# Performance work log

Hardware: AMD Instinct MI355X
Metric: run time of the kernel (lower is better)

## Reference

```python
import jax, jax.numpy as jnp
import numpy as np

B, L, C, H, FF = 2, 2048, 1024, 16, 4096
HD = C // H
SCALE = HD ** -0.5
EPS = 1e-5


def _ln(x, g, b):
    m = jnp.mean(x, axis=-1, keepdims=True)
    v = jnp.mean((x - m) ** 2, axis=-1, keepdims=True)
    return (x - m) * jax.lax.rsqrt(v + EPS) * g + b


def setup_inputs() -> dict:
    key = jax.random.key(0)
    ks = jax.random.split(key, 12)
    s = lambda fan_in: 1.0 / np.sqrt(fan_in)
    return {
        "x": jax.random.normal(ks[0], (B, L, C), jnp.float32),
        "freq_diff": jax.random.normal(ks[1], (B, L), jnp.float32),
        "qkv_w": jax.random.normal(ks[2], (C, 3 * C), jnp.float32) * s(C),
        "qkv_b": jnp.zeros((3 * C,), jnp.float32),
        "fp_w1": jax.random.normal(ks[3], (1, C), jnp.float32),
        "fp_b1": jnp.zeros((C,), jnp.float32),
        "fp_ln_g": jnp.ones((C,), jnp.float32),
        "fp_ln_b": jnp.zeros((C,), jnp.float32),
        "fp_w2": jax.random.normal(ks[4], (C, C), jnp.float32) * s(C),
        "fp_b2": jnp.zeros((C,), jnp.float32),
        "wq_w": jax.random.normal(ks[5], (HD, HD), jnp.float32) * s(HD),
        "wq_b": jnp.zeros((HD,), jnp.float32),
        "wk_w": jax.random.normal(ks[6], (HD, HD), jnp.float32) * s(HD),
        "wk_b": jnp.zeros((HD,), jnp.float32),
        "out_w": jax.random.normal(ks[7], (C, C), jnp.float32) * s(C),
        "out_b": jnp.zeros((C,), jnp.float32),
        "n1_g": jnp.ones((C,), jnp.float32),
        "n1_b": jnp.zeros((C,), jnp.float32),
        "n2_g": jnp.ones((C,), jnp.float32),
        "n2_b": jnp.zeros((C,), jnp.float32),
        "mlp_w1": jax.random.normal(ks[8], (C, FF), jnp.float32) * s(C),
        "mlp_b1": jnp.zeros((FF,), jnp.float32),
        "mlp_w2": jax.random.normal(ks[9], (FF, C), jnp.float32) * s(FF),
        "mlp_b2": jnp.zeros((C,), jnp.float32),
        "freq_scale": jnp.ones((1,), jnp.float32),
    }


def reference(x, freq_diff, qkv_w, qkv_b, fp_w1, fp_b1, fp_ln_g, fp_ln_b,
              fp_w2, fp_b2, wq_w, wq_b, wk_w, wk_b, out_w, out_b,
              n1_g, n1_b, n2_g, n2_b, mlp_w1, mlp_b1, mlp_w2, mlp_b2,
              freq_scale):
    shortcut = x
    xn = _ln(x, n1_g, n1_b)
    qkv = (xn @ qkv_w + qkv_b).reshape(B, L, 3, H, HD)
    qkv = jnp.transpose(qkv, (2, 0, 3, 1, 4))  # [3,B,H,L,HD]
    q, k, v = qkv[0], qkv[1], qkv[2]

    # frequency bias: MLP on scalar freq_diff -> per-head bias vectors
    fb = freq_diff[..., None] @ fp_w1 + fp_b1          # [B,L,C]
    fb = jax.nn.gelu(_ln(fb, fp_ln_g, fp_ln_b), approximate=False)
    fb = fb @ fp_w2 + fp_b2                            # [B,L,C]
    fb = jnp.transpose(fb.reshape(B, L, H, HD), (0, 2, 1, 3))  # [B,H,L,HD]
    qb = fb @ wq_w + wq_b
    kb = fb @ wk_w + wk_b
    freq_attn_bias = jnp.einsum('bhqd,bhkd->bhqk', qb, kb)

    attn = jnp.einsum('bhqd,bhkd->bhqk', q, k) * SCALE
    attn = attn + freq_scale[0] * freq_attn_bias
    attn = jax.nn.softmax(attn, axis=-1)
    o = jnp.einsum('bhqk,bhkd->bhqd', attn, v)
    o = jnp.transpose(o, (0, 2, 1, 3)).reshape(B, L, C)
    x = shortcut + (o @ out_w + out_b)

    xn2 = _ln(x, n2_g, n2_b)
    h = jax.nn.gelu(xn2 @ mlp_w1 + mlp_b1, approximate=False)
    x = x + (h @ mlp_w2 + mlp_b2)
    return x
```

## Files before the change

kernel.cpp:

```cpp
#include <hip/hip_runtime.h>
#include <math.h>


typedef __bf16 bf16;
typedef float f32x4 __attribute__((ext_vector_type(4)));
typedef bf16 bf16x8 __attribute__((ext_vector_type(8)));
typedef bf16 bf16x4 __attribute__((ext_vector_type(4)));

#define DEVINL __device__ __forceinline__

#define LOG2E 1.4426950408889634f

DEVINL float fast_exp2(float x) { return __builtin_amdgcn_exp2f(x); }

DEVINL void async_load16(const void* g, void* l) {
  __builtin_amdgcn_global_load_lds(
      (const __attribute__((address_space(1))) unsigned int*)g,
      (__attribute__((address_space(3))) unsigned int*)l, 16, 0, 0);
}

DEVINL f32x4 mfma16(bf16x8 a, bf16x8 b, f32x4 c) {
  return __builtin_amdgcn_mfma_f32_16x16x32_bf16(a, b, c, 0, 0, 0);
}

DEVINL float gelu_exact(float v) {
  return 0.5f * v * (1.0f + erff(v * 0.70710678118654752f));
}

DEVINL void block_reduce2(float& a, float& b, float* red, int tid) {
#pragma unroll
  for (int off = 32; off >= 1; off >>= 1) {
    a += __shfl_xor(a, off);
    b += __shfl_xor(b, off);
  }
  int w = tid >> 6;
  if ((tid & 63) == 0) { red[2 * w] = a; red[2 * w + 1] = b; }
  __syncthreads();
  a = red[0] + red[2] + red[4] + red[6];
  b = red[1] + red[3] + red[5] + red[7];
  __syncthreads();
}

__global__ __launch_bounds__(256) void transpose_cast(
    const float* __restrict__ W, bf16* __restrict__ Wt, int K, int N) {
  __shared__ float tile[32][33];
  int n0 = blockIdx.x * 32, k0 = blockIdx.y * 32;
  int tx = threadIdx.x & 31, ty = threadIdx.x >> 5;
#pragma unroll
  for (int r = 0; r < 4; ++r)
    tile[ty + r * 8][tx] = W[(size_t)(k0 + ty + r * 8) * N + n0 + tx];
  __syncthreads();
#pragma unroll
  for (int r = 0; r < 4; ++r)
    Wt[(size_t)(n0 + ty + r * 8) * K + k0 + tx] = (bf16)tile[tx][ty + r * 8];
}

__global__ __launch_bounds__(256) void prec_qk(
    const float* __restrict__ fp_w2, const float* __restrict__ fp_b2,
    const float* __restrict__ wq_w, const float* __restrict__ wq_b,
    const float* __restrict__ wk_w, const float* __restrict__ wk_b,
    bf16* __restrict__ wqk2t, float* __restrict__ bqk) {
  __shared__ float Wl[64 * 64];
  __shared__ float Al[64 * 128];
  const int id = blockIdx.x;
  const int sel = id >> 7, h = (id >> 3) & 15, ck = id & 7;
  const int t = threadIdx.x;
  const float* wsel = sel ? wk_w : wq_w;
#pragma unroll
  for (int i = 0; i < 4; ++i)
    ((float4*)Wl)[i * 256 + t] = ((const float4*)wsel)[i * 256 + t];
  const int c0 = ck * 128, off = h * 64;
#pragma unroll
  for (int it = 0; it < 8; ++it) {
    int idx = it * 256 + t;
    int rr = idx >> 4, c4 = idx & 15;
    float4 v = *(const float4*)(fp_w2 + (size_t)(c0 + rr) * 1024 + off + c4 * 4);
    float vv[4] = {v.x, v.y, v.z, v.w};
#pragma unroll
    for (int k = 0; k < 4; ++k) {
      int i2 = c4 * 4 + k;
      Al[i2 * 128 + (rr ^ (i2 & 31))] = vv[k];
    }
  }
  __syncthreads();
  const int cr = t & 127, jh = (t >> 7) * 32;
  float acc[32];
#pragma unroll
  for (int j = 0; j < 32; ++j) acc[j] = 0.f;
  for (int i = 0; i < 64; ++i) {
    float a = Al[i * 128 + (cr ^ (i & 31))];
    const float4* wrow = (const float4*)(Wl + i * 64 + jh);
#pragma unroll
    for (int j4 = 0; j4 < 8; ++j4) {
      float4 wv = wrow[j4];
      acc[j4 * 4 + 0] += a * wv.x;
      acc[j4 * 4 + 1] += a * wv.y;
      acc[j4 * 4 + 2] += a * wv.z;
      acc[j4 * 4 + 3] += a * wv.w;
    }
  }
  const int nbase = sel * 1024 + off + jh;
#pragma unroll
  for (int j = 0; j < 32; ++j)
    wqk2t[(size_t)(nbase + j) * 1024 + c0 + cr] = (bf16)acc[j];
  if (ck == 0 && t < 64) {
    float s = 0.f;
    for (int i = 0; i < 64; ++i) s += fp_b2[off + i] * Wl[i * 64 + t];
    bqk[sel * 1024 + off + t] = s + (sel ? wk_b[t] : wq_b[t]);
  }
}

__global__ __launch_bounds__(256) void ln1_kernel(
    const float* __restrict__ x, const float* __restrict__ fd,
    const float* __restrict__ g1, const float* __restrict__ b1,
    const float* __restrict__ fw1, const float* __restrict__ fb1,
    const float* __restrict__ flg, const float* __restrict__ flb,
    bf16* __restrict__ xn, bf16* __restrict__ gout) {
  __shared__ float red[8];
  int tok = blockIdx.x, t = threadIdx.x;
  float4 xv = ((const float4*)(x + (size_t)tok * 1024))[t];
  float s = xv.x + xv.y + xv.z + xv.w;
  float ss = xv.x * xv.x + xv.y * xv.y + xv.z * xv.z + xv.w * xv.w;
  block_reduce2(s, ss, red, t);
  float mean = s * (1.0f / 1024.0f);
  float rsig = rsqrtf(ss * (1.0f / 1024.0f) - mean * mean + 1e-5f);
  float4 g4 = ((const float4*)g1)[t], b4 = ((const float4*)b1)[t];
  bf16x4 o;
  o[0] = (bf16)((xv.x - mean) * rsig * g4.x + b4.x);
  o[1] = (bf16)((xv.y - mean) * rsig * g4.y + b4.y);
  o[2] = (bf16)((xv.z - mean) * rsig * g4.z + b4.z);
  o[3] = (bf16)((xv.w - mean) * rsig * g4.w + b4.w);
  ((bf16x4*)xn)[(size_t)tok * 256 + t] = o;

  float dv = fd[tok];
  float4 w4 = ((const float4*)fw1)[t], c4 = ((const float4*)fb1)[t];
  float f0 = dv * w4.x + c4.x, f1 = dv * w4.y + c4.y;
  float f2 = dv * w4.z + c4.z, f3 = dv * w4.w + c4.w;
  s = f0 + f1 + f2 + f3;
  ss = f0 * f0 + f1 * f1 + f2 * f2 + f3 * f3;
  block_reduce2(s, ss, red, t);
  mean = s * (1.0f / 1024.0f);
  rsig = rsqrtf(ss * (1.0f / 1024.0f) - mean * mean + 1e-5f);
  float4 lg = ((const float4*)flg)[t], lb = ((const float4*)flb)[t];
  bf16x4 q;
  q[0] = (bf16)gelu_exact((f0 - mean) * rsig * lg.x + lb.x);
  q[1] = (bf16)gelu_exact((f1 - mean) * rsig * lg.y + lb.y);
  q[2] = (bf16)gelu_exact((f2 - mean) * rsig * lg.z + lb.z);
  q[3] = (bf16)gelu_exact((f3 - mean) * rsig * lg.w + lb.w);
  ((bf16x4*)gout)[(size_t)tok * 256 + t] = q;
}

__global__ __launch_bounds__(256) void ln_kernel(
    const float* __restrict__ xin, const float* __restrict__ g,
    const float* __restrict__ b, bf16* __restrict__ xout) {
  __shared__ float red[8];
  int tok = blockIdx.x, t = threadIdx.x;
  float4 xv = ((const float4*)(xin + (size_t)tok * 1024))[t];
  float s = xv.x + xv.y + xv.z + xv.w;
  float ss = xv.x * xv.x + xv.y * xv.y + xv.z * xv.z + xv.w * xv.w;
  block_reduce2(s, ss, red, t);
  float mean = s * (1.0f / 1024.0f);
  float rsig = rsqrtf(ss * (1.0f / 1024.0f) - mean * mean + 1e-5f);
  float4 g4 = ((const float4*)g)[t], b4 = ((const float4*)b)[t];
  bf16x4 o;
  o[0] = (bf16)((xv.x - mean) * rsig * g4.x + b4.x);
  o[1] = (bf16)((xv.y - mean) * rsig * g4.y + b4.y);
  o[2] = (bf16)((xv.z - mean) * rsig * g4.z + b4.z);
  o[3] = (bf16)((xv.w - mean) * rsig * g4.w + b4.w);
  ((bf16x4*)xout)[(size_t)tok * 256 + t] = o;
}

template <class Epi>
__global__ __launch_bounds__(256) void gemm_bf16_k(
    const bf16* __restrict__ A, const bf16* __restrict__ Bt,
    int M, int N, int K, Epi epi) {
  __shared__ bf16 As[2][128 * 32];
  __shared__ bf16 Bs[2][128 * 32];
  const int tid = threadIdx.x;
  const int lane = tid & 63, w = tid >> 6;
  const int quad = lane >> 4, lm = lane & 15;
  const int wm = w >> 1, wn = w & 1;
  const int m0 = blockIdx.y * 128, n0 = blockIdx.x * 128;

  f32x4 acc[4][4];
#pragma unroll
  for (int i = 0; i < 4; ++i)
#pragma unroll
    for (int j = 0; j < 4; ++j) {
      acc[i][j][0] = 0.f; acc[i][j][1] = 0.f; acc[i][j][2] = 0.f; acc[i][j][3] = 0.f;
    }

  const bf16* Ag = A + (size_t)m0 * K;
  const bf16* Bg = Bt + (size_t)n0 * K;

  auto stage = [&](int k0, int buf) {
#pragma unroll
    for (int i = 0; i < 2; ++i) {
      int ch = i * 256 + tid, r = ch >> 2, c = ch & 3;
      async_load16(Ag + (size_t)r * K + k0 + c * 8,
                   (char*)As[buf] + (i * 256 + w * 64) * 16);
      async_load16(Bg + (size_t)r * K + k0 + c * 8,
                   (char*)Bs[buf] + (i * 256 + w * 64) * 16);
    }
  };

  stage(0, 0);
  const int nk = K >> 5;
  for (int ki = 0; ki < nk; ++ki) {
    __syncthreads();
    if (ki + 1 < nk) stage((ki + 1) << 5, (ki + 1) & 1);
    const bf16* Ac = As[ki & 1];
    const bf16* Bc = Bs[ki & 1];
    bf16x8 af[4], bfv[4];
#pragma unroll
    for (int mi = 0; mi < 4; ++mi)
      af[mi] = *(const bf16x8*)(Ac + (wm * 64 + mi * 16 + lm) * 32 + quad * 8);
#pragma unroll
    for (int ni = 0; ni < 4; ++ni)
      bfv[ni] = *(const bf16x8*)(Bc + (wn * 64 + ni * 16 + lm) * 32 + quad * 8);
#pragma unroll
    for (int mi = 0; mi < 4; ++mi)
#pragma unroll
      for (int ni = 0; ni < 4; ++ni)
        acc[mi][ni] = mfma16(af[mi], bfv[ni], acc[mi][ni]);
  }

#pragma unroll
  for (int mi = 0; mi < 4; ++mi)
#pragma unroll
    for (int ni = 0; ni < 4; ++ni)
      epi(m0 + wm * 64 + mi * 16 + quad * 4, n0 + wn * 64 + ni * 16 + lm, acc[mi][ni]);
}

__global__ __launch_bounds__(256) void gemm_mlp2_part(
    const bf16* __restrict__ A, const bf16* __restrict__ Bt,
    float* __restrict__ part) {
  __shared__ bf16 As[2][128 * 32];
  __shared__ bf16 Bs[2][128 * 32];
  const int tid = threadIdx.x;
  const int lane = tid & 63, w = tid >> 6;
  const int quad = lane >> 4, lm = lane & 15;
  const int wm = w >> 1, wn = w & 1;
  const int id = blockIdx.x;
  const int kz = id & 3;
  const int n0 = ((id >> 2) & 7) * 128;
  const int m0 = (id >> 5) * 128;

  f32x4 acc[4][4];
#pragma unroll
  for (int i = 0; i < 4; ++i)
#pragma unroll
    for (int j = 0; j < 4; ++j) {
      acc[i][j][0] = 0.f; acc[i][j][1] = 0.f; acc[i][j][2] = 0.f; acc[i][j][3] = 0.f;
    }

  const bf16* Ag = A + (size_t)m0 * 4096 + kz * 1024;
  const bf16* Bg = Bt + (size_t)n0 * 4096 + kz * 1024;

  auto stage = [&](int k0, int buf) {
#pragma unroll
    for (int i = 0; i < 2; ++i) {
      int ch = i * 256 + tid, r = ch >> 2, c = ch & 3;
      async_load16(Ag + (size_t)r * 4096 + k0 + c * 8,
                   (char*)As[buf] + (i * 256 + w * 64) * 16);
      async_load16(Bg + (size_t)r * 4096 + k0 + c * 8,
                   (char*)Bs[buf] + (i * 256 + w * 64) * 16);
    }
  };

  stage(0, 0);
  for (int ki = 0; ki < 32; ++ki) {
    __syncthreads();
    if (ki + 1 < 32) stage((ki + 1) << 5, (ki + 1) & 1);
    const bf16* Ac = As[ki & 1];
    const bf16* Bc = Bs[ki & 1];
    bf16x8 af[4], bfv[4];
#pragma unroll
    for (int mi = 0; mi < 4; ++mi)
      af[mi] = *(const bf16x8*)(Ac + (wm * 64 + mi * 16 + lm) * 32 + quad * 8);
#pragma unroll
    for (int ni = 0; ni < 4; ++ni)
      bfv[ni] = *(const bf16x8*)(Bc + (wn * 64 + ni * 16 + lm) * 32 + quad * 8);
#pragma unroll
    for (int mi = 0; mi < 4; ++mi)
#pragma unroll
      for (int ni = 0; ni < 4; ++ni)
        acc[mi][ni] = mfma16(af[mi], bfv[ni], acc[mi][ni]);
  }

  float* dst = part + (size_t)kz * 4096 * 1024;
#pragma unroll
  for (int mi = 0; mi < 4; ++mi)
#pragma unroll
    for (int ni = 0; ni < 4; ++ni) {
      int row = m0 + wm * 64 + mi * 16 + quad * 4;
      int col = n0 + wn * 64 + ni * 16 + lm;
#pragma unroll
      for (int r = 0; r < 4; ++r)
        dst[(size_t)(row + r) * 1024 + col] = acc[mi][ni][r];
    }
}

__global__ __launch_bounds__(256) void reduce_mlp2(
    const float* __restrict__ part, float* __restrict__ out) {
  size_t i = (size_t)blockIdx.x * 256 + threadIdx.x;
  const float4* p = (const float4*)part;
  float4 o = ((const float4*)out)[i];
  const size_t S = (size_t)4096 * 256;
  float4 a = p[i], b = p[i + S], c = p[i + 2 * S], d = p[i + 3 * S];
  o.x += a.x + b.x + c.x + d.x;
  o.y += a.y + b.y + c.y + d.y;
  o.z += a.z + b.z + c.z + d.z;
  o.w += a.w + b.w + c.w + d.w;
  ((float4*)out)[i] = o;
}

struct EpiQKV {
  const float* __restrict__ bias;
  bf16 *Qc, *Kc, *Vt;
  DEVINL void operator()(int row, int col, f32x4 v) const {
    int b = row >> 11, l = row & 2047;
    float bia = bias[col];
    if (col < 1024) {
      int h = col >> 6, d = col & 63;
      bf16* p = Qc + (size_t)(((b << 4) + h) * 2048 + l) * 128 + d;
#pragma unroll
      for (int r = 0; r < 4; ++r) p[r * 128] = (bf16)((v[r] + bia) * (0.125f * LOG2E));
    } else if (col < 2048) {
      int c2 = col - 1024, h = c2 >> 6, d = c2 & 63;
      bf16* p = Kc + (size_t)(((b << 4) + h) * 2048 + l) * 128 + d;
#pragma unroll
      for (int r = 0; r < 4; ++r) p[r * 128] = (bf16)(v[r] + bia);
    } else {
      int c2 = col - 2048, h = c2 >> 6, d = c2 & 63;
      bf16x4 pk;
#pragma unroll
      for (int r = 0; r < 4; ++r) pk[r] = (bf16)(v[r] + bia);
      *(bf16x4*)(Vt + (size_t)(((b << 4) + h) * 64 + d) * 2048 + l) = pk;
    }
  }
};

struct EpiQBKB {
  const float* __restrict__ bias;
  const float* __restrict__ fs;
  bf16 *Qc, *Kc;
  DEVINL void operator()(int row, int col, f32x4 v) const {
    int b = row >> 11, l = row & 2047;
    float bia = bias[col];
    if (col < 1024) {
      int h = col >> 6, d = col & 63;
      float sc = fs[0] * LOG2E;
      bf16* p = Qc + (size_t)(((b << 4) + h) * 2048 + l) * 128 + 64 + d;
#pragma unroll
      for (int r = 0; r < 4; ++r) p[r * 128] = (bf16)((v[r] + bia) * sc);
    } else {
      int c2 = col - 1024, h = c2 >> 6, d = c2 & 63;
      bf16* p = Kc + (size_t)(((b << 4) + h) * 2048 + l) * 128 + 64 + d;
#pragma unroll
      for (int r = 0; r < 4; ++r) p[r * 128] = (bf16)(v[r] + bia);
    }
  }
};

struct EpiOut {
  const float* __restrict__ bias;
  const float* __restrict__ x;
  const float* __restrict__ b2;
  float* x1;
  float* out0;
  DEVINL void operator()(int row, int col, f32x4 v) const {
    float bia = bias[col];
    float b2v = b2[col];
#pragma unroll
    for (int r = 0; r < 4; ++r) {
      size_t idx = (size_t)(row + r) * 1024 + col;
      float xv = x[idx] + v[r] + bia;
      x1[idx] = xv;
      out0[idx] = xv + b2v;
    }
  }
};

struct EpiMLP1 {
  const float* __restrict__ bias;
  bf16* hbf;
  DEVINL void operator()(int row, int col, f32x4 v) const {
    float bia = bias[col];
#pragma unroll
    for (int r = 0; r < 4; ++r)
      hbf[(size_t)(row + r) * 4096 + col] = (bf16)gelu_exact(v[r] + bia);
  }
};

__global__ __launch_bounds__(512, 4) void flash_kernel(
    const bf16* __restrict__ Qc, const bf16* __restrict__ Kcp,
    const bf16* __restrict__ Vt, bf16* __restrict__ Obf) {
  __shared__ bf16 KsA[64 * 128];
  __shared__ bf16 KsB[64 * 128];
  __shared__ bf16 VsA[64 * 64];
  __shared__ bf16 VsB[64 * 64];
  __shared__ bf16 Ps[128 * 64];

  const int tid = threadIdx.x, lane = tid & 63, w = tid >> 6;
  const int quad = lane >> 4, lm = lane & 15;
  const int id = blockIdx.x;
  const int bh = id & 31, qt = id >> 5;
  const int b = bh >> 4, h = bh & 15;

  const bf16* Qg = Qc + ((size_t)bh * 2048 + qt * 128) * 128;
#pragma unroll
  for (int i = 0; i < 4; ++i) {
    int ch = i * 512 + tid, r = ch >> 4, cs = ch & 15, c = cs ^ (r & 7);
    char* dst = (i < 2) ? (char*)KsA + (i * 512 + w * 64) * 16
                        : (char*)KsB + ((i - 2) * 512 + w * 64) * 16;
    async_load16(Qg + (size_t)r * 128 + c * 8, dst);
  }
  __syncthreads();
  const int qr = w * 16 + lm;
  bf16x8 qf[4];
  {
    const bf16* base = (w < 4) ? KsA : KsB;
    int rr = qr & 63;
#pragma unroll
    for (int ks = 0; ks < 4; ++ks) {
      int pos = (ks * 4 + quad) ^ (lm & 7);
      qf[ks] = *(const bf16x8*)(base + rr * 128 + pos * 8);
    }
  }
  __syncthreads();

  float m_run = -3.0e38f, l_run = 0.f;
  f32x4 o_acc[4];
#pragma unroll
  for (int nf = 0; nf < 4; ++nf) {
    o_acc[nf][0] = 0.f; o_acc[nf][1] = 0.f; o_acc[nf][2] = 0.f; o_acc[nf][3] = 0.f;
  }

  const bf16* Kg0 = Kcp + (size_t)bh * 2048 * 128;
  const bf16* Vg0 = Vt + (size_t)bh * 64 * 2048;

  auto stage = [&](int kv, bf16* Kdst, bf16* Vdst) {
    const bf16* Kg = Kg0 + (size_t)kv * 64 * 128;
#pragma unroll
    for (int i = 0; i < 2; ++i) {
      int ch = i * 512 + tid, key = ch >> 4, c = (ch & 15) ^ (key & 7);
      async_load16(Kg + (size_t)key * 128 + c * 8,
                   (char*)Kdst + (i * 512 + w * 64) * 16);
    }
    {
      int d = tid >> 3, c = (tid & 7) ^ (d & 7);
      async_load16(Vg0 + (size_t)d * 2048 + kv * 64 + c * 8,
                   (char*)Vdst + (w * 64) * 16);
    }
  };

  stage(0, KsA, VsA);

  for (int kv = 0; kv < 32; ++kv) {
    const bf16* Kcur = (kv & 1) ? KsB : KsA;
    const bf16* Vcur = (kv & 1) ? VsB : VsA;
    __syncthreads();
    if (kv + 1 < 32)
      stage(kv + 1, (kv & 1) ? KsA : KsB, (kv & 1) ? VsA : VsB);

    f32x4 sa[4];
#pragma unroll
    for (int nk = 0; nk < 4; ++nk) {
      sa[nk][0] = 0.f; sa[nk][1] = 0.f; sa[nk][2] = 0.f; sa[nk][3] = 0.f;
    }
#pragma unroll
    for (int ks = 0; ks < 4; ++ks) {
      bf16x8 ak[4];
#pragma unroll
      for (int nk = 0; nk < 4; ++nk) {
        int key = nk * 16 + lm;
        int pos = (ks * 4 + quad) ^ (key & 7);
        ak[nk] = *(const bf16x8*)(Kcur + key * 128 + pos * 8);
      }
#pragma unroll
      for (int nk = 0; nk < 4; ++nk)
        sa[nk] = mfma16(ak[nk], qf[ks], sa[nk]);
    }

    float mx = sa[0][0];
#pragma unroll
    for (int nk = 0; nk < 4; ++nk)
#pragma unroll
      for (int rg = 0; rg < 4; ++rg) mx = fmaxf(mx, sa[nk][rg]);
    mx = fmaxf(mx, __shfl_xor(mx, 16));
    mx = fmaxf(mx, __shfl_xor(mx, 32));
    float mnew = fmaxf(m_run, mx);
    float alpha = fast_exp2(m_run - mnew);
    m_run = mnew;
    float rs = 0.f;
#pragma unroll
    for (int nk = 0; nk < 4; ++nk)
#pragma unroll
      for (int rg = 0; rg < 4; ++rg) {
        float pv = fast_exp2(sa[nk][rg] - mnew);
        sa[nk][rg] = pv;
        rs += pv;
      }
    rs += __shfl_xor(rs, 16);
    rs += __shfl_xor(rs, 32);
    l_run = l_run * alpha + rs;
#pragma unroll
    for (int nf = 0; nf < 4; ++nf) {
      o_acc[nf][0] *= alpha; o_acc[nf][1] *= alpha;
      o_acc[nf][2] *= alpha; o_acc[nf][3] *= alpha;
    }

#pragma unroll
    for (int nk = 0; nk < 4; ++nk) {
      int c16 = 2 * nk + (quad >> 1);
      int cs = c16 ^ (lm & 7);
      bf16x4 pk;
      pk[0] = (bf16)sa[nk][0]; pk[1] = (bf16)sa[nk][1];
      pk[2] = (bf16)sa[nk][2]; pk[3] = (bf16)sa[nk][3];
      *(bf16x4*)(Ps + qr * 64 + cs * 8 + (quad & 1) * 4) = pk;
    }

#pragma unroll
    for (int ks = 0; ks < 2; ++ks) {
      bf16x8 pa, vb[4];
      {
        int cs = (ks * 4 + quad) ^ (lm & 7);
        pa = *(const bf16x8*)(Ps + qr * 64 + cs * 8);
      }
#pragma unroll
      for (int nf = 0; nf < 4; ++nf) {
        int d = nf * 16 + lm;
        int cs = (ks * 4 + quad) ^ (d & 7);
        vb[nf] = *(const bf16x8*)(Vcur + d * 64 + cs * 8);
      }
#pragma unroll
      for (int nf = 0; nf < 4; ++nf)
        o_acc[nf] = mfma16(vb[nf], pa, o_acc[nf]);
    }
  }

  float inv = 1.0f / l_run;
  int l = qt * 128 + qr;
#pragma unroll
  for (int nf = 0; nf < 4; ++nf) {
    bf16x4 ov;
#pragma unroll
    for (int rg = 0; rg < 4; ++rg) ov[rg] = (bf16)(o_acc[nf][rg] * inv);
    int d = h * 64 + nf * 16 + quad * 4;
    *(bf16x4*)(Obf + ((size_t)b * 2048 + l) * 1024 + d) = ov;
  }
}

extern "C" void kernel_launch(void* const* d_in, const int* in_sizes, int n_in,
                              void* d_out, int out_size, void* d_ws, size_t ws_size,
                              hipStream_t stream) {
  (void)in_sizes; (void)n_in; (void)out_size; (void)ws_size;
  const float* x      = (const float*)d_in[0];
  const float* fd     = (const float*)d_in[1];
  const float* qkv_w  = (const float*)d_in[2];
  const float* qkv_b  = (const float*)d_in[3];
  const float* fp_w1  = (const float*)d_in[4];
  const float* fp_b1  = (const float*)d_in[5];
  const float* fp_ln_g= (const float*)d_in[6];
  const float* fp_ln_b= (const float*)d_in[7];
  const float* fp_w2  = (const float*)d_in[8];
  const float* fp_b2  = (const float*)d_in[9];
  const float* wq_w   = (const float*)d_in[10];
  const float* wq_b   = (const float*)d_in[11];
  const float* wk_w   = (const float*)d_in[12];
  const float* wk_b   = (const float*)d_in[13];
  const float* out_w  = (const float*)d_in[14];
  const float* out_b  = (const float*)d_in[15];
  const float* n1_g   = (const float*)d_in[16];
  const float* n1_b   = (const float*)d_in[17];
  const float* n2_g   = (const float*)d_in[18];
  const float* n2_b   = (const float*)d_in[19];
  const float* mlp_w1 = (const float*)d_in[20];
  const float* mlp_b1 = (const float*)d_in[21];
  const float* mlp_w2 = (const float*)d_in[22];
  const float* mlp_b2 = (const float*)d_in[23];
  const float* fscale = (const float*)d_in[24];
  float* out = (float*)d_out;

  char* p = (char*)d_ws;
  auto take = [&](size_t n) { char* r = p; p += (n + 255) & ~(size_t)255; return r; };
  bf16* xn_bf  = (bf16*)take((size_t)4096 * 1024 * 2);
  bf16* g_bf   = (bf16*)take((size_t)4096 * 1024 * 2);
  bf16* Qc     = (bf16*)take((size_t)32 * 2048 * 128 * 2);
  bf16* Kc     = (bf16*)take((size_t)32 * 2048 * 128 * 2);
  bf16* Vt     = (bf16*)take((size_t)32 * 64 * 2048 * 2);
  bf16* o_bf   = (bf16*)take((size_t)4096 * 1024 * 2);
  float* x1    = (float*)take((size_t)4096 * 1024 * 4);
  bf16* ln2_bf = (bf16*)take((size_t)4096 * 1024 * 2);
  bf16* h_bf   = (bf16*)take((size_t)4096 * 4096 * 2);
  bf16* qkv_wt = (bf16*)take((size_t)3072 * 1024 * 2);
  bf16* out_wt = (bf16*)take((size_t)1024 * 1024 * 2);
  bf16* w1t    = (bf16*)take((size_t)4096 * 1024 * 2);
  bf16* w2t    = (bf16*)take((size_t)1024 * 4096 * 2);
  bf16* wqk2t  = (bf16*)take((size_t)2048 * 1024 * 2);
  float* bqk   = (float*)take((size_t)2048 * 4);

  float* part = (float*)xn_bf;

  dim3 b256(256);

  transpose_cast<<<dim3(3072 / 32, 1024 / 32), b256, 0, stream>>>(qkv_w, qkv_wt, 1024, 3072);
  transpose_cast<<<dim3(1024 / 32, 1024 / 32), b256, 0, stream>>>(out_w, out_wt, 1024, 1024);
  transpose_cast<<<dim3(4096 / 32, 1024 / 32), b256, 0, stream>>>(mlp_w1, w1t, 1024, 4096);
  transpose_cast<<<dim3(1024 / 32, 4096 / 32), b256, 0, stream>>>(mlp_w2, w2t, 4096, 1024);
  prec_qk<<<dim3(256), b256, 0, stream>>>(fp_w2, fp_b2, wq_w, wq_b, wk_w, wk_b, wqk2t, bqk);

  ln1_kernel<<<dim3(4096), b256, 0, stream>>>(x, fd, n1_g, n1_b, fp_w1, fp_b1,
                                              fp_ln_g, fp_ln_b, xn_bf, g_bf);

  gemm_bf16_k<<<dim3(24, 32), b256, 0, stream>>>(xn_bf, qkv_wt, 4096, 3072, 1024,
                                                 EpiQKV{qkv_b, Qc, Kc, Vt});
  gemm_bf16_k<<<dim3(16, 32), b256, 0, stream>>>(g_bf, wqk2t, 4096, 2048, 1024,
                                                 EpiQBKB{bqk, fscale, Qc, Kc});
  flash_kernel<<<dim3(512), dim3(512), 0, stream>>>(Qc, Kc, Vt, o_bf);

  gemm_bf16_k<<<dim3(8, 32), b256, 0, stream>>>(o_bf, out_wt, 4096, 1024, 1024,
                                                EpiOut{out_b, x, mlp_b2, x1, out});
  ln_kernel<<<dim3(4096), b256, 0, stream>>>(x1, n2_g, n2_b, ln2_bf);
  gemm_bf16_k<<<dim3(32, 32), b256, 0, stream>>>(ln2_bf, w1t, 4096, 4096, 1024,
                                                 EpiMLP1{mlp_b1, h_bf});
  gemm_mlp2_part<<<dim3(1024), b256, 0, stream>>>(h_bf, w2t, part);
  reduce_mlp2<<<dim3(4096), b256, 0, stream>>>(part, out);
}
```

Measured before the change: 513.9 us.

## Add 256x256 ping-pong GEMM with swizzled LDS and use for QKV/MLP GEMMs

Introduces a 512-thread 256x256-tile bf16 GEMM kernel with XOR-swizzled LDS layout, four-phase interleaved async staging, raw barriers with MFMA priority bumps and explicit vmcnt waits, plus block-index swizzling for L2 locality. It replaces the 128x128 GEMMs for QKV, freq-bias QK, MLP1 and split-K MLP2. The goal is higher data reuse per tile, fewer LDS bank conflicts and better overlap of loads with MFMA. In exchange, small grids (128-256 blocks) may underfill the GPU's compute units, and the hand-placed waitcnt sequencing is fragile.

```diff
diff --git a/kernel.cpp b/kernel.cpp
--- a/kernel.cpp
+++ b/kernel.cpp
@@ -25,6 +25,12 @@
 
 DEVINL float gelu_exact(float v) {
   return 0.5f * v * (1.0f + erff(v * 0.70710678118654752f));
+}
+
+DEVINL void hard_barrier() {
+  asm volatile("" ::: "memory");
+  __builtin_amdgcn_s_barrier();
+  asm volatile("" ::: "memory");
 }
 
 DEVINL void block_reduce2(float& a, float& b, float* red, int tid) {
@@ -170,6 +176,131 @@
   ((bf16x4*)xout)[(size_t)tok * 256 + t] = o;
 }
 
+#define PHASE(MH, NH, LA, LB, STAGE_STMT, WAIT_STMT)                          \
+  do {                                                                        \
+    if (LA) {                                                                 \
+      _Pragma("unroll") for (int ml = 0; ml < 4; ++ml) {                      \
+        _Pragma("unroll") for (int ks = 0; ks < 2; ++ks) {                    \
+          const int rr = ml * 16 + lm;                                        \
+          const int cc = (((ks * 4 + quad) ^ (lm & 7)) << 3);                 \
+          af[ml][ks] = *(const bf16x8*)&As[bsel][MH][wm][rr][cc];             \
+        }                                                                     \
+      }                                                                       \
+    }                                                                         \
+    if (LB) {                                                                 \
+      _Pragma("unroll") for (int nl = 0; nl < 2; ++nl) {                      \
+        _Pragma("unroll") for (int ks = 0; ks < 2; ++ks) {                    \
+          const int rr = nl * 16 + lm;                                        \
+          const int cc = (((ks * 4 + quad) ^ (lm & 7)) << 3);                 \
+          bfr[nl][ks] = *(const bf16x8*)&Bs[bsel][NH][wn][rr][cc];            \
+        }                                                                     \
+      }                                                                       \
+    }                                                                         \
+    STAGE_STMT;                                                               \
+    hard_barrier();                                                           \
+    __builtin_amdgcn_s_setprio(1);                                            \
+    _Pragma("unroll") for (int ks = 0; ks < 2; ++ks) {                        \
+      _Pragma("unroll") for (int ml = 0; ml < 4; ++ml) {                      \
+        _Pragma("unroll") for (int nl = 0; nl < 2; ++nl) {                    \
+          acc[(MH)*4 + ml][(NH)*2 + nl] = mfma16(                             \
+              af[ml][ks], bfr[nl][ks], acc[(MH)*4 + ml][(NH)*2 + nl]);        \
+        }                                                                     \
+      }                                                                       \
+    }                                                                         \
+    __builtin_amdgcn_s_setprio(0);                                            \
+    WAIT_STMT;                                                                \
+    hard_barrier();                                                           \
+  } while (0)
+
+template <class Epi>
+__global__ __launch_bounds__(512, 2) void gemm256(
+    const bf16* __restrict__ A, const bf16* __restrict__ Bt,
+    int lda, int ldb, int K, int kstride, int nbx, int nblk, int rowoffz,
+    Epi epi) {
+  __shared__ __align__(16) bf16 As[2][2][2][64][64];
+  __shared__ __align__(16) bf16 Bs[2][2][4][32][64];
+
+  const int tid = threadIdx.x;
+  const int lane = tid & 63, w = tid >> 6;
+  const int quad = lane >> 4, lm = lane & 15;
+  const int wm = w >> 2, wn = w & 3;
+
+  const int kz = blockIdx.x / nblk;
+  const int bid = blockIdx.x - kz * nblk;
+  const int swz = (nblk & 7) ? bid : ((bid & 7) * (nblk >> 3) + (bid >> 3));
+  const int tm = swz / nbx, tn = swz - tm * nbx;
+  const int m0 = tm << 8, n0 = tn << 8;
+  const int rowoff = kz * rowoffz;
+  A += (size_t)kz * kstride;
+  Bt += (size_t)kz * kstride;
+
+  const bf16* Abase = A + (size_t)m0 * lda;
+  const bf16* Bbase = Bt + (size_t)n0 * ldb;
+
+  auto stageA = [&](int b, int mh, int kt) {
+#pragma unroll
+    for (int j = 0; j < 2; ++j) {
+      const int q = (w * 2 + j) * 64 + lane;
+      const int wm2 = q >> 9, rr = (q >> 3) & 63, c = q & 7;
+      async_load16(Abase + (size_t)(wm2 * 128 + mh * 64 + rr) * lda +
+                       (size_t)kt * 64 + ((c ^ (rr & 7)) << 3),
+                   (char*)&As[b][mh][0][0][0] + (w * 2 + j) * 1024);
+    }
+  };
+  auto stageB = [&](int b, int nh, int kt) {
+#pragma unroll
+    for (int j = 0; j < 2; ++j) {
+      const int q = (w * 2 + j) * 64 + lane;
+      const int wn4 = q >> 8, rr = (q >> 3) & 31, c = q & 7;
+      async_load16(Bbase + (size_t)(wn4 * 64 + nh * 32 + rr) * ldb +
+                       (size_t)kt * 64 + ((c ^ (rr & 7)) << 3),
+                   (char*)&Bs[b][nh][0][0][0] + (w * 2 + j) * 1024);
+    }
+  };
+
+  f32x4 acc[8][4];
+#pragma unroll
+  for (int i = 0; i < 8; ++i)
+#pragma unroll
+    for (int j = 0; j < 4; ++j) {
+      acc[i][j][0] = 0.f; acc[i][j][1] = 0.f;
+      acc[i][j][2] = 0.f; acc[i][j][3] = 0.f;
+    }
+  bf16x8 af[4][2], bfr[2][2];
+
+  stageA(0, 0, 0);
+  stageB(0, 1, 0);
+  stageA(0, 1, 0);
+  stageB(0, 0, 0);
+  stageA(1, 0, 1);
+  stageB(1, 1, 1);
+  asm volatile("s_waitcnt vmcnt(4)" ::: "memory");
+  hard_barrier();
+
+  const int nt = K >> 6;
+  int bsel = 0;
+  for (int t = 0; t < nt; ++t, bsel ^= 1) {
+    PHASE(0, 0, 1, 1, { if (t + 1 < nt) stageA(bsel ^ 1, 1, t + 1); }, {});
+    PHASE(0, 1, 0, 1, { if (t + 1 < nt) stageB(bsel ^ 1, 0, t + 1); }, {});
+    PHASE(1, 1, 1, 0, { if (t + 2 < nt) stageA(bsel, 0, t + 2); }, {});
+    PHASE(1, 0, 0, 1, { if (t + 2 < nt) stageB(bsel, 1, t + 2); },
+          {
+            if (t + 2 < nt) {
+              asm volatile("s_waitcnt vmcnt(4)" ::: "memory");
+            } else if (t + 1 < nt) {
+              asm volatile("s_waitcnt vmcnt(0)" ::: "memory");
+            }
+          });
+  }
+
+#pragma unroll
+  for (int mi = 0; mi < 8; ++mi)
+#pragma unroll
+    for (int ni = 0; ni < 4; ++ni)
+      epi(rowoff + m0 + wm * 128 + mi * 16 + quad * 4,
+          n0 + wn * 64 + ni * 16 + lm, acc[mi][ni]);
+}
+
 template <class Epi>
 __global__ __launch_bounds__(256) void gemm_bf16_k(
     const bf16* __restrict__ A, const bf16* __restrict__ Bt,
@@ -230,75 +361,6 @@
 #pragma unroll
     for (int ni = 0; ni < 4; ++ni)
       epi(m0 + wm * 64 + mi * 16 + quad * 4, n0 + wn * 64 + ni * 16 + lm, acc[mi][ni]);
-}
-
-__global__ __launch_bounds__(256) void gemm_mlp2_part(
-    const bf16* __restrict__ A, const bf16* __restrict__ Bt,
-    float* __restrict__ part) {
-  __shared__ bf16 As[2][128 * 32];
-  __shared__ bf16 Bs[2][128 * 32];
-  const int tid = threadIdx.x;
-  const int lane = tid & 63, w = tid >> 6;
-  const int quad = lane >> 4, lm = lane & 15;
-  const int wm = w >> 1, wn = w & 1;
-  const int id = blockIdx.x;
-  const int kz = id & 3;
-  const int n0 = ((id >> 2) & 7) * 128;
-  const int m0 = (id >> 5) * 128;
-
-  f32x4 acc[4][4];
-#pragma unroll
-  for (int i = 0; i < 4; ++i)
-#pragma unroll
-    for (int j = 0; j < 4; ++j) {
-      acc[i][j][0] = 0.f; acc[i][j][1] = 0.f; acc[i][j][2] = 0.f; acc[i][j][3] = 0.f;
-    }
-
-  const bf16* Ag = A + (size_t)m0 * 4096 + kz * 1024;
-  const bf16* Bg = Bt + (size_t)n0 * 4096 + kz * 1024;
-
-  auto stage = [&](int k0, int buf) {
-#pragma unroll
-    for (int i = 0; i < 2; ++i) {
-      int ch = i * 256 + tid, r = ch >> 2, c = ch & 3;
-      async_load16(Ag + (size_t)r * 4096 + k0 + c * 8,
-                   (char*)As[buf] + (i * 256 + w * 64) * 16);
-      async_load16(Bg + (size_t)r * 4096 + k0 + c * 8,
-                   (char*)Bs[buf] + (i * 256 + w * 64) * 16);
-    }
-  };
-
-  stage(0, 0);
-  for (int ki = 0; ki < 32; ++ki) {
-    __syncthreads();
-    if (ki + 1 < 32) stage((ki + 1) << 5, (ki + 1) & 1);
-    const bf16* Ac = As[ki & 1];
-    const bf16* Bc = Bs[ki & 1];
-    bf16x8 af[4], bfv[4];
-#pragma unroll
-    for (int mi = 0; mi < 4; ++mi)
-      af[mi] = *(const bf16x8*)(Ac + (wm * 64 + mi * 16 + lm) * 32 + quad * 8);
-#pragma unroll
-    for (int ni = 0; ni < 4; ++ni)
-      bfv[ni] = *(const bf16x8*)(Bc + (wn * 64 + ni * 16 + lm) * 32 + quad * 8);
-#pragma unroll
-    for (int mi = 0; mi < 4; ++mi)
-#pragma unroll
-      for (int ni = 0; ni < 4; ++ni)
-        acc[mi][ni] = mfma16(af[mi], bfv[ni], acc[mi][ni]);
-  }
-
-  float* dst = part + (size_t)kz * 4096 * 1024;
-#pragma unroll
-  for (int mi = 0; mi < 4; ++mi)
-#pragma unroll
-    for (int ni = 0; ni < 4; ++ni) {
-      int row = m0 + wm * 64 + mi * 16 + quad * 4;
-      int col = n0 + wn * 64 + ni * 16 + lm;
-#pragma unroll
-      for (int r = 0; r < 4; ++r)
-        dst[(size_t)(row + r) * 1024 + col] = acc[mi][ni][r];
-    }
 }
 
 __global__ __launch_bounds__(256) void reduce_mlp2(
@@ -390,6 +452,15 @@
 #pragma unroll
     for (int r = 0; r < 4; ++r)
       hbf[(size_t)(row + r) * 4096 + col] = (bf16)gelu_exact(v[r] + bia);
+  }
+};
+
+struct EpiPart {
+  float* part;
+  DEVINL void operator()(int row, int col, f32x4 v) const {
+#pragma unroll
+    for (int r = 0; r < 4; ++r)
+      part[(size_t)(row + r) * 1024 + col] = v[r];
   }
 };
 
@@ -603,7 +674,7 @@
 
   float* part = (float*)xn_bf;
 
-  dim3 b256(256);
+  dim3 b256(256), b512(512);
 
   transpose_cast<<<dim3(3072 / 32, 1024 / 32), b256, 0, stream>>>(qkv_w, qkv_wt, 1024, 3072);
   transpose_cast<<<dim3(1024 / 32, 1024 / 32), b256, 0, stream>>>(out_w, out_wt, 1024, 1024);
@@ -614,17 +685,18 @@
   ln1_kernel<<<dim3(4096), b256, 0, stream>>>(x, fd, n1_g, n1_b, fp_w1, fp_b1,
                                               fp_ln_g, fp_ln_b, xn_bf, g_bf);
 
-  gemm_bf16_k<<<dim3(24, 32), b256, 0, stream>>>(xn_bf, qkv_wt, 4096, 3072, 1024,
-                                                 EpiQKV{qkv_b, Qc, Kc, Vt});
-  gemm_bf16_k<<<dim3(16, 32), b256, 0, stream>>>(g_bf, wqk2t, 4096, 2048, 1024,
-                                                 EpiQBKB{bqk, fscale, Qc, Kc});
+  gemm256<<<dim3(192), b512, 0, stream>>>(xn_bf, qkv_wt, 1024, 1024, 1024, 0,
+                                          12, 192, 0, EpiQKV{qkv_b, Qc, Kc, Vt});
+  gemm256<<<dim3(128), b512, 0, stream>>>(g_bf, wqk2t, 1024, 1024, 1024, 0,
+                                          8, 128, 0, EpiQBKB{bqk, fscale, Qc, Kc});
   flash_kernel<<<dim3(512), dim3(512), 0, stream>>>(Qc, Kc, Vt, o_bf);
 
   gemm_bf16_k<<<dim3(8, 32), b256, 0, stream>>>(o_bf, out_wt, 4096, 1024, 1024,
                                                 EpiOut{out_b, x, mlp_b2, x1, out});
   ln_kernel<<<dim3(4096), b256, 0, stream>>>(x1, n2_g, n2_b, ln2_bf);
-  gemm_bf16_k<<<dim3(32, 32), b256, 0, stream>>>(ln2_bf, w1t, 4096, 4096, 1024,
-                                                 EpiMLP1{mlp_b1, h_bf});
-  gemm_mlp2_part<<<dim3(1024), b256, 0, stream>>>(h_bf, w2t, part);
+  gemm256<<<dim3(256), b512, 0, stream>>>(ln2_bf, w1t, 1024, 1024, 1024, 0,
+                                          16, 256, 0, EpiMLP1{mlp_b1, h_bf});
+  gemm256<<<dim3(256), b512, 0, stream>>>(h_bf, w2t, 4096, 4096, 1024, 1024,
+                                          4, 64, 4096, EpiPart{part});
   reduce_mlp2<<<dim3(4096), b256, 0, stream>>>(part, out);
 }
```

After: 489.0 us. 4.8% less time.
